# Kernel tuning notes

Measured on AMD Instinct MI355X. Metric: run time of the kernel, lower is better.

Reference implementation:

```python
import jax, jax.numpy as jnp
import numpy as np
import math

IN_DIM = 512
PARAM_DIM = 512
OUT_DIM = 2048
GROUPS = 4
COMPRESS = 4
PLANES = OUT_DIM // COMPRESS          # 512
GROUP_PLANES = PLANES // GROUPS       # 128
ATTN_SCALE = PLANES ** (-0.5)         # note: full planes, as in the source
N, L = 16, 1024
M = L  # required by sv.reshape(N, planes, L)


def equal_linear(x, w, b, in_dim):
    # EqualLinear: F.linear(x, w * (1/sqrt(in_dim)) * lr_mul, bias * lr_mul), lr_mul=1
    scale = 1.0 / math.sqrt(in_dim)
    return jnp.einsum('nlc,oc->nlo', x, w * scale) + b


def setup_inputs() -> dict:
    key = jax.random.key(0)
    ks = jax.random.split(key, 8)
    return {
        'attention': jax.random.normal(ks[0], (N, L, IN_DIM), dtype=jnp.float32),
        'op_param': jax.random.normal(ks[1], (N, M, PARAM_DIM), dtype=jnp.float32),
        'q_w': jax.random.normal(ks[2], (PLANES, PARAM_DIM), dtype=jnp.float32),
        'q_b': jnp.zeros((PLANES,), dtype=jnp.float32),
        'k_w': jax.random.normal(ks[3], (PLANES, IN_DIM), dtype=jnp.float32),
        'k_b': jnp.zeros((PLANES,), dtype=jnp.float32),
        'v_w': jax.random.normal(ks[4], (PLANES, IN_DIM), dtype=jnp.float32),
        'v_b': jnp.zeros((PLANES,), dtype=jnp.float32),
        'proj_w': jax.random.normal(ks[5], (OUT_DIM, PLANES), dtype=jnp.float32),
        'proj_b': jnp.zeros((OUT_DIM,), dtype=jnp.float32),
    }


def reference(attention, op_param, q_w, q_b, k_w, k_b, v_w, v_b, proj_w, proj_b):
    n, l, _ = attention.shape
    m = op_param.shape[1]
    # q/k/v: (N, T, planes) -> (N, groups, group_planes, T)
    q = equal_linear(op_param, q_w, q_b, PARAM_DIM).reshape(n, m, GROUPS, GROUP_PLANES).transpose(0, 2, 3, 1)
    k = equal_linear(attention, k_w, k_b, IN_DIM).reshape(n, l, GROUPS, GROUP_PLANES).transpose(0, 2, 3, 1)
    v = equal_linear(attention, v_w, v_b, IN_DIM).reshape(n, l, GROUPS, GROUP_PLANES).transpose(0, 2, 3, 1)
    # scores: (N, groups, M, L)
    qk = jnp.einsum('ngdm,ngdl->ngml', q, k) * ATTN_SCALE
    sim = jax.nn.softmax(qk, axis=3)
    # sv: (N, groups, group_planes, M)
    sv = jnp.einsum('ngml,ngdl->ngdm', sim, v)
    # (N, planes, L) -> (N, L, planes); valid because M == L
    stacked = sv.reshape(n, PLANES, l).transpose(0, 2, 1)
    out = equal_linear(stacked, proj_w, proj_b, PLANES)
    return out
```

## Files before the change

kernel.cpp:

```cpp
#include <hip/hip_runtime.h>
#include <hip/hip_bf16.h>

#define NB 16
#define TT 1024
#define CC 512
#define PP 512
#define GG 4
#define DD 128
#define OO 2048

#define SCL 0.04419417382415922f

typedef __attribute__((ext_vector_type(8))) short short8;
typedef __attribute__((ext_vector_type(4))) float floatx4;
#define MFMA(a, b, c) __builtin_amdgcn_mfma_f32_16x16x32_bf16((a), (b), (c), 0, 0, 0)

static __device__ __forceinline__ float bf2f(unsigned short u) {
  union { unsigned int i; float f; } v; v.i = ((unsigned int)u) << 16; return v.f;
}
static __device__ __forceinline__ unsigned short f2bf(float f) {
  __hip_bfloat16 h = __float2bfloat16(f);
  return *reinterpret_cast<unsigned short*>(&h);
}
static __device__ __forceinline__ ushort4 pack4(float4 v) {
  ushort4 o; o.x = f2bf(v.x); o.y = f2bf(v.y); o.z = f2bf(v.z); o.w = f2bf(v.w); return o;
}

template <int VLAY>
__global__ __launch_bounds__(256) void k_proj(
    const float* __restrict__ x, const float* __restrict__ w,
    const float* __restrict__ b, unsigned short* __restrict__ y) {
  __shared__ unsigned short Aw[128][32];
  __shared__ unsigned short Xw[128][32];
  const int n  = blockIdx.z;
  const int p0 = blockIdx.y * 128;
  const int t0 = blockIdx.x * 128;
  const int tid  = threadIdx.x;
  const int wave = tid >> 6, lane = tid & 63;
  const int l15  = lane & 15, quad = lane >> 4;
  const int wm = (wave >> 1) * 64, wn = (wave & 1) * 64;
  const int srow = tid >> 3, scol = (tid & 7) * 4;
  const float* xn = x + (size_t)n * TT * CC;
  floatx4 acc[4][4] = {};

  for (int k0 = 0; k0 < CC; k0 += 32) {
    float4 aw[4], ax[4];
#pragma unroll
    for (int q = 0; q < 4; ++q) {
      aw[q] = *reinterpret_cast<const float4*>(w  + (size_t)(p0 + srow + q * 32) * CC + k0 + scol);
      ax[q] = *reinterpret_cast<const float4*>(xn + (size_t)(t0 + srow + q * 32) * CC + k0 + scol);
    }
    __syncthreads();
#pragma unroll
    for (int q = 0; q < 4; ++q) {
      *reinterpret_cast<ushort4*>(&Aw[srow + q * 32][scol]) = pack4(aw[q]);
      *reinterpret_cast<ushort4*>(&Xw[srow + q * 32][scol]) = pack4(ax[q]);
    }
    __syncthreads();
    short8 af[4], bx[4];
#pragma unroll
    for (int mt = 0; mt < 4; ++mt)
      af[mt] = *reinterpret_cast<const short8*>(&Aw[wm + mt * 16 + l15][quad * 8]);
#pragma unroll
    for (int nt = 0; nt < 4; ++nt)
      bx[nt] = *reinterpret_cast<const short8*>(&Xw[wn + nt * 16 + l15][quad * 8]);
#pragma unroll
    for (int mt = 0; mt < 4; ++mt)
#pragma unroll
      for (int nt = 0; nt < 4; ++nt)
        acc[mt][nt] = MFMA(af[mt], bx[nt], acc[mt][nt]);
  }

#pragma unroll
  for (int mt = 0; mt < 4; ++mt) {
    const int pb = p0 + wm + mt * 16 + quad * 4;
    const float4 bias = *reinterpret_cast<const float4*>(b + pb);
    const float bb[4] = {bias.x, bias.y, bias.z, bias.w};
#pragma unroll
    for (int nt = 0; nt < 4; ++nt) {
      const int tc = t0 + wn + nt * 16 + l15;
      if (VLAY == 0) {
        ushort4 o;
        o.x = f2bf(acc[mt][nt][0] * SCL + bb[0]);
        o.y = f2bf(acc[mt][nt][1] * SCL + bb[1]);
        o.z = f2bf(acc[mt][nt][2] * SCL + bb[2]);
        o.w = f2bf(acc[mt][nt][3] * SCL + bb[3]);
        *reinterpret_cast<ushort4*>(y + ((size_t)n * TT + tc) * PP + pb) = o;
      } else {
#pragma unroll
        for (int r = 0; r < 4; ++r)
          y[((size_t)n * PP + pb + r) * TT + tc] = f2bf(acc[mt][nt][r] * SCL + bb[r]);
      }
    }
  }
}

__global__ __launch_bounds__(256, 2) void k_attn(
    const unsigned short* __restrict__ Q,
    const unsigned short* __restrict__ K,
    const unsigned short* __restrict__ V,
    unsigned short* __restrict__ SV) {
  __shared__ unsigned short Sc[32][1032];
  __shared__ float rowinv[32];
  const int lin = blockIdx.x;
  const int wu  = (lin >> 3) | ((lin & 7) << 8);
  const int m0 = (wu & 31) * 32;
  const int g  = (wu >> 5) & 3;
  const int n  = wu >> 7;
  const int tid  = threadIdx.x;
  const int wave = tid >> 6, lane = tid & 63;
  const int l15  = lane & 15, quad = lane >> 4;

  const unsigned short* Qn = Q + (size_t)n * TT * PP;
  const unsigned short* Kn = K + (size_t)n * TT * PP;
  const unsigned short* Vn = V + ((size_t)n * PP + g * DD) * TT;

  short8 aq[2][4];
#pragma unroll
  for (int mt = 0; mt < 2; ++mt)
#pragma unroll
    for (int ds = 0; ds < 4; ++ds)
      aq[mt][ds] = *reinterpret_cast<const short8*>(
          Qn + (size_t)(m0 + mt * 16 + l15) * PP + g * DD + ds * 32 + quad * 8);

  auto kload = [&](short8 (&dst)[4][4], int base_l) {
#pragma unroll
    for (int ds = 0; ds < 4; ++ds)
#pragma unroll
      for (int j = 0; j < 4; ++j)
        dst[ds][j] = *reinterpret_cast<const short8*>(
            Kn + (size_t)(base_l + (wave * 4 + j) * 16 + l15) * PP +
            g * DD + ds * 32 + quad * 8);
  };
  auto kcomp = [&](const short8 (&bk)[4][4], int base_l) {
    floatx4 acc[2][4] = {};
#pragma unroll
    for (int ds = 0; ds < 4; ++ds)
#pragma unroll
      for (int j = 0; j < 4; ++j) {
        acc[0][j] = MFMA(aq[0][ds], bk[ds][j], acc[0][j]);
        acc[1][j] = MFMA(aq[1][ds], bk[ds][j], acc[1][j]);
      }
#pragma unroll
    for (int mt = 0; mt < 2; ++mt)
#pragma unroll
      for (int j = 0; j < 4; ++j) {
        const int lc = base_l + (wave * 4 + j) * 16 + l15;
#pragma unroll
        for (int r = 0; r < 4; ++r)
          Sc[mt * 16 + quad * 4 + r][lc] = f2bf(acc[mt][j][r] * SCL);
      }
  };

  short8 bkA[4][4], bkB[4][4];
  kload(bkA, 0);
  kload(bkB, 256);
  kcomp(bkA, 0);
  kload(bkA, 512);
  kcomp(bkB, 256);
  kload(bkB, 768);
  kcomp(bkA, 512);
  kcomp(bkB, 768);
  __syncthreads();

  {
    const int mi = tid >> 3;
    const int j  = tid & 7;
    unsigned short* row = &Sc[mi][0];
    float mx = -1e30f;
#pragma unroll
    for (int i = 0; i < 16; ++i) {
      short8 u = *reinterpret_cast<const short8*>(&row[(i * 8 + j) * 8]);
      float a0 = fmaxf(bf2f((unsigned short)u[0]), bf2f((unsigned short)u[1]));
      float a1 = fmaxf(bf2f((unsigned short)u[2]), bf2f((unsigned short)u[3]));
      float a2 = fmaxf(bf2f((unsigned short)u[4]), bf2f((unsigned short)u[5]));
      float a3 = fmaxf(bf2f((unsigned short)u[6]), bf2f((unsigned short)u[7]));
      mx = fmaxf(mx, fmaxf(fmaxf(a0, a1), fmaxf(a2, a3)));
    }
#pragma unroll
    for (int off = 4; off; off >>= 1) mx = fmaxf(mx, __shfl_xor(mx, off, 8));
    float sum = 0.f;
#pragma unroll
    for (int i = 0; i < 16; ++i) {
      short8 u = *reinterpret_cast<short8*>(&row[(i * 8 + j) * 8]);
      short8 o;
      float s0 = 0.f, s1 = 0.f;
#pragma unroll
      for (int e = 0; e < 8; e += 2) {
        float e0 = __expf(bf2f((unsigned short)u[e])     - mx);
        float e1 = __expf(bf2f((unsigned short)u[e + 1]) - mx);
        s0 += e0; s1 += e1;
        o[e]     = (short)f2bf(e0);
        o[e + 1] = (short)f2bf(e1);
      }
      sum += s0 + s1;
      *reinterpret_cast<short8*>(&row[(i * 8 + j) * 8]) = o;
    }
#pragma unroll
    for (int off = 4; off; off >>= 1) sum += __shfl_xor(sum, off, 8);
    if (j == 0) rowinv[mi] = 1.f / sum;
  }
  __syncthreads();

  floatx4 av[2][2] = {};
  auto vload = [&](short8 (&dst)[2], int ls) {
#pragma unroll
    for (int a = 0; a < 2; ++a)
      dst[a] = *reinterpret_cast<const short8*>(
          Vn + (size_t)(wave * 32 + a * 16 + l15) * TT + ls * 32 + quad * 8);
  };
  auto vstep = [&](const short8 (&va)[2], int ls) {
    short8 bp[2];
#pragma unroll
    for (int mt = 0; mt < 2; ++mt)
      bp[mt] = *reinterpret_cast<const short8*>(&Sc[mt * 16 + l15][ls * 32 + quad * 8]);
#pragma unroll
    for (int a = 0; a < 2; ++a)
#pragma unroll
      for (int mt = 0; mt < 2; ++mt)
        av[a][mt] = MFMA(va[a], bp[mt], av[a][mt]);
  };

  short8 va0[2], va1[2], va2[2], va3[2];
  vload(va0, 0); vload(va1, 1); vload(va2, 2); vload(va3, 3);
#pragma unroll
  for (int ls = 0; ls < 32; ls += 4) {
    vstep(va0, ls);     if (ls + 4 < 32) vload(va0, ls + 4);
    vstep(va1, ls + 1); if (ls + 5 < 32) vload(va1, ls + 5);
    vstep(va2, ls + 2); if (ls + 6 < 32) vload(va2, ls + 6);
    vstep(va3, ls + 3); if (ls + 7 < 32) vload(va3, ls + 7);
  }

#pragma unroll
  for (int a = 0; a < 2; ++a) {
    const int pb = g * DD + wave * 32 + a * 16 + quad * 4;
#pragma unroll
    for (int mt = 0; mt < 2; ++mt) {
      const float inv = rowinv[mt * 16 + l15];
      ushort4 o;
      o.x = f2bf(av[a][mt][0] * inv);
      o.y = f2bf(av[a][mt][1] * inv);
      o.z = f2bf(av[a][mt][2] * inv);
      o.w = f2bf(av[a][mt][3] * inv);
      *reinterpret_cast<ushort4*>(
          SV + ((size_t)n * TT + m0 + mt * 16 + l15) * PP + pb) = o;
    }
  }
}

__global__ __launch_bounds__(256) void k_out(
    const unsigned short* __restrict__ SVp, const float* __restrict__ w,
    const float* __restrict__ b, float* __restrict__ out) {
  __shared__ unsigned short Wt[128][32];
  __shared__ unsigned short St[128][32];
  const int n  = blockIdx.z;
  const int o0 = blockIdx.y * 128;
  const int t0 = blockIdx.x * 128;
  const int tid  = threadIdx.x;
  const int wave = tid >> 6, lane = tid & 63;
  const int l15  = lane & 15, quad = lane >> 4;
  const int wm = (wave >> 1) * 64, wn = (wave & 1) * 64;
  const int srow = tid >> 3, scol = (tid & 7) * 4;
  const unsigned short* SVn = SVp + (size_t)n * TT * PP;
  floatx4 acc[4][4] = {};

  for (int k0 = 0; k0 < PP; k0 += 32) {
    float4 awf[4];
    ushort4 us[4];
#pragma unroll
    for (int q = 0; q < 4; ++q) {
      awf[q] = *reinterpret_cast<const float4*>(w + (size_t)(o0 + srow + q * 32) * PP + k0 + scol);
      us[q]  = *reinterpret_cast<const ushort4*>(SVn + (size_t)(t0 + srow + q * 32) * PP + k0 + scol);
    }
    __syncthreads();
#pragma unroll
    for (int q = 0; q < 4; ++q) {
      *reinterpret_cast<ushort4*>(&Wt[srow + q * 32][scol]) = pack4(awf[q]);
      *reinterpret_cast<ushort4*>(&St[srow + q * 32][scol]) = us[q];
    }
    __syncthreads();
    short8 af[4], bs[4];
#pragma unroll
    for (int mt = 0; mt < 4; ++mt)
      af[mt] = *reinterpret_cast<const short8*>(&Wt[wm + mt * 16 + l15][quad * 8]);
#pragma unroll
    for (int nt = 0; nt < 4; ++nt)
      bs[nt] = *reinterpret_cast<const short8*>(&St[wn + nt * 16 + l15][quad * 8]);
#pragma unroll
    for (int mt = 0; mt < 4; ++mt)
#pragma unroll
      for (int nt = 0; nt < 4; ++nt)
        acc[mt][nt] = MFMA(af[mt], bs[nt], acc[mt][nt]);
  }

#pragma unroll
  for (int mt = 0; mt < 4; ++mt) {
    const int ob = o0 + wm + mt * 16 + quad * 4;
    const float4 bias = *reinterpret_cast<const float4*>(b + ob);
    const float bb[4] = {bias.x, bias.y, bias.z, bias.w};
#pragma unroll
    for (int nt = 0; nt < 4; ++nt) {
      const int tc = t0 + wn + nt * 16 + l15;
      float4 o;
      o.x = acc[mt][nt][0] * SCL + bb[0];
      o.y = acc[mt][nt][1] * SCL + bb[1];
      o.z = acc[mt][nt][2] * SCL + bb[2];
      o.w = acc[mt][nt][3] * SCL + bb[3];
      *reinterpret_cast<float4*>(out + ((size_t)n * TT + tc) * OO + ob) = o;
    }
  }
}

extern "C" void kernel_launch(void* const* d_in, const int* in_sizes, int n_in,
                              void* d_out, int out_size, void* d_ws, size_t ws_size,
                              hipStream_t stream) {
  (void)in_sizes; (void)n_in; (void)out_size; (void)ws_size;
  const float* attention = (const float*)d_in[0];
  const float* op_param  = (const float*)d_in[1];
  const float* q_w = (const float*)d_in[2];
  const float* q_b = (const float*)d_in[3];
  const float* k_w = (const float*)d_in[4];
  const float* k_b = (const float*)d_in[5];
  const float* v_w = (const float*)d_in[6];
  const float* v_b = (const float*)d_in[7];
  const float* proj_w = (const float*)d_in[8];
  const float* proj_b = (const float*)d_in[9];
  float* out = (float*)d_out;

  const size_t NPT = (size_t)NB * PP * TT;
  unsigned short* scratch = (unsigned short*)d_out;
  unsigned short* Qw  = scratch;
  unsigned short* Kw  = scratch + NPT;
  unsigned short* Vw  = scratch + 2 * NPT;
  unsigned short* SVw = (unsigned short*)d_ws;

  dim3 blk(256);
  dim3 gp(TT / 128, PP / 128, NB);
  k_proj<0><<<gp, blk, 0, stream>>>(op_param,  q_w, q_b, Qw);
  k_proj<0><<<gp, blk, 0, stream>>>(attention, k_w, k_b, Kw);
  k_proj<1><<<gp, blk, 0, stream>>>(attention, v_w, v_b, Vw);
  k_attn<<<dim3(2048), blk, 0, stream>>>(Qw, Kw, Vw, SVw);
  k_out<<<dim3(TT / 128, OO / 128, NB), blk, 0, stream>>>(SVw, proj_w, proj_b, out);
}
```

Measured before the change: 447.1 us.

## Enlarge attention tile to 64 query rows with 512-thread blocks

The attention kernel now handles 64 query rows per block with 8 waves instead of 32 rows with 4 waves. This doubles reuse of each loaded K/V fragment across query rows and halves the grid. The K loop now covers all 1024 keys in two 512-key chunks. The float-to-bf16 conversion is replaced by a manual round-to-nearest-even bit trick. In exchange, register pressure rises sharply under the 512,2 launch bounds, which risks spills, and the 132 KB shared score buffer limits occupancy to one block per CU.

Measured after the change: 418.3 us. -6.4%, faster.

```diff
diff --git a/kernel.cpp b/kernel.cpp
--- a/kernel.cpp
+++ b/kernel.cpp
@@ -19,8 +19,9 @@
   union { unsigned int i; float f; } v; v.i = ((unsigned int)u) << 16; return v.f;
 }
 static __device__ __forceinline__ unsigned short f2bf(float f) {
-  __hip_bfloat16 h = __float2bfloat16(f);
-  return *reinterpret_cast<unsigned short*>(&h);
+  union { float f; unsigned int i; } v; v.f = f;
+  unsigned int r = (v.i + 0x7fffu + ((v.i >> 16) & 1u)) >> 16;
+  return (unsigned short)r;
 }
 static __device__ __forceinline__ ushort4 pack4(float4 v) {
   ushort4 o; o.x = f2bf(v.x); o.y = f2bf(v.y); o.z = f2bf(v.z); o.w = f2bf(v.w); return o;
@@ -95,18 +96,18 @@
   }
 }
 
-__global__ __launch_bounds__(256, 2) void k_attn(
+__global__ __launch_bounds__(512, 2) void k_attn(
     const unsigned short* __restrict__ Q,
     const unsigned short* __restrict__ K,
     const unsigned short* __restrict__ V,
     unsigned short* __restrict__ SV) {
-  __shared__ unsigned short Sc[32][1032];
-  __shared__ float rowinv[32];
+  __shared__ unsigned short Sc[64][1032];
+  __shared__ float rowinv[64];
   const int lin = blockIdx.x;
-  const int wu  = (lin >> 3) | ((lin & 7) << 8);
-  const int m0 = (wu & 31) * 32;
-  const int g  = (wu >> 5) & 3;
-  const int n  = wu >> 7;
+  const int wu  = (lin >> 3) | ((lin & 7) << 7);
+  const int m0 = (wu & 15) * 64;
+  const int g  = (wu >> 4) & 3;
+  const int n  = wu >> 6;
   const int tid  = threadIdx.x;
   const int wave = tid >> 6, lane = tid & 63;
   const int l15  = lane & 15, quad = lane >> 4;
@@ -115,9 +116,9 @@
   const unsigned short* Kn = K + (size_t)n * TT * PP;
   const unsigned short* Vn = V + ((size_t)n * PP + g * DD) * TT;
 
-  short8 aq[2][4];
-#pragma unroll
-  for (int mt = 0; mt < 2; ++mt)
+  short8 aq[4][4];
+#pragma unroll
+  for (int mt = 0; mt < 4; ++mt)
 #pragma unroll
     for (int ds = 0; ds < 4; ++ds)
       aq[mt][ds] = *reinterpret_cast<const short8*>(
@@ -133,16 +134,16 @@
             g * DD + ds * 32 + quad * 8);
   };
   auto kcomp = [&](const short8 (&bk)[4][4], int base_l) {
-    floatx4 acc[2][4] = {};
+    floatx4 acc[4][4] = {};
 #pragma unroll
     for (int ds = 0; ds < 4; ++ds)
 #pragma unroll
-      for (int j = 0; j < 4; ++j) {
-        acc[0][j] = MFMA(aq[0][ds], bk[ds][j], acc[0][j]);
-        acc[1][j] = MFMA(aq[1][ds], bk[ds][j], acc[1][j]);
-      }
-#pragma unroll
-    for (int mt = 0; mt < 2; ++mt)
+      for (int j = 0; j < 4; ++j)
+#pragma unroll
+        for (int mt = 0; mt < 4; ++mt)
+          acc[mt][j] = MFMA(aq[mt][ds], bk[ds][j], acc[mt][j]);
+#pragma unroll
+    for (int mt = 0; mt < 4; ++mt)
 #pragma unroll
       for (int j = 0; j < 4; ++j) {
         const int lc = base_l + (wave * 4 + j) * 16 + l15;
@@ -154,13 +155,9 @@
 
   short8 bkA[4][4], bkB[4][4];
   kload(bkA, 0);
-  kload(bkB, 256);
+  kload(bkB, 512);
   kcomp(bkA, 0);
-  kload(bkA, 512);
-  kcomp(bkB, 256);
-  kload(bkB, 768);
-  kcomp(bkA, 512);
-  kcomp(bkB, 768);
+  kcomp(bkB, 512);
   __syncthreads();
 
   {
@@ -202,49 +199,39 @@
   }
   __syncthreads();
 
-  floatx4 av[2][2] = {};
-  auto vload = [&](short8 (&dst)[2], int ls) {
-#pragma unroll
-    for (int a = 0; a < 2; ++a)
-      dst[a] = *reinterpret_cast<const short8*>(
-          Vn + (size_t)(wave * 32 + a * 16 + l15) * TT + ls * 32 + quad * 8);
+  floatx4 av[4] = {};
+  auto vload = [&](int ls) {
+    return *reinterpret_cast<const short8*>(
+        Vn + (size_t)(wave * 16 + l15) * TT + ls * 32 + quad * 8);
   };
-  auto vstep = [&](const short8 (&va)[2], int ls) {
-    short8 bp[2];
-#pragma unroll
-    for (int mt = 0; mt < 2; ++mt)
-      bp[mt] = *reinterpret_cast<const short8*>(&Sc[mt * 16 + l15][ls * 32 + quad * 8]);
-#pragma unroll
-    for (int a = 0; a < 2; ++a)
-#pragma unroll
-      for (int mt = 0; mt < 2; ++mt)
-        av[a][mt] = MFMA(va[a], bp[mt], av[a][mt]);
+  auto vstep = [&](short8 va, int ls) {
+#pragma unroll
+    for (int mt = 0; mt < 4; ++mt) {
+      short8 bp = *reinterpret_cast<const short8*>(&Sc[mt * 16 + l15][ls * 32 + quad * 8]);
+      av[mt] = MFMA(va, bp, av[mt]);
+    }
   };
 
-  short8 va0[2], va1[2], va2[2], va3[2];
-  vload(va0, 0); vload(va1, 1); vload(va2, 2); vload(va3, 3);
+  short8 va0 = vload(0), va1 = vload(1), va2 = vload(2), va3 = vload(3);
 #pragma unroll
   for (int ls = 0; ls < 32; ls += 4) {
-    vstep(va0, ls);     if (ls + 4 < 32) vload(va0, ls + 4);
-    vstep(va1, ls + 1); if (ls + 5 < 32) vload(va1, ls + 5);
-    vstep(va2, ls + 2); if (ls + 6 < 32) vload(va2, ls + 6);
-    vstep(va3, ls + 3); if (ls + 7 < 32) vload(va3, ls + 7);
-  }
-
-#pragma unroll
-  for (int a = 0; a < 2; ++a) {
-    const int pb = g * DD + wave * 32 + a * 16 + quad * 4;
-#pragma unroll
-    for (int mt = 0; mt < 2; ++mt) {
-      const float inv = rowinv[mt * 16 + l15];
-      ushort4 o;
-      o.x = f2bf(av[a][mt][0] * inv);
-      o.y = f2bf(av[a][mt][1] * inv);
-      o.z = f2bf(av[a][mt][2] * inv);
-      o.w = f2bf(av[a][mt][3] * inv);
-      *reinterpret_cast<ushort4*>(
-          SV + ((size_t)n * TT + m0 + mt * 16 + l15) * PP + pb) = o;
-    }
+    vstep(va0, ls);     if (ls + 4 < 32) va0 = vload(ls + 4);
+    vstep(va1, ls + 1); if (ls + 5 < 32) va1 = vload(ls + 5);
+    vstep(va2, ls + 2); if (ls + 6 < 32) va2 = vload(ls + 6);
+    vstep(va3, ls + 3); if (ls + 7 < 32) va3 = vload(ls + 7);
+  }
+
+  const int pb = g * DD + wave * 16 + quad * 4;
+#pragma unroll
+  for (int mt = 0; mt < 4; ++mt) {
+    const float inv = rowinv[mt * 16 + l15];
+    ushort4 o;
+    o.x = f2bf(av[mt][0] * inv);
+    o.y = f2bf(av[mt][1] * inv);
+    o.z = f2bf(av[mt][2] * inv);
+    o.w = f2bf(av[mt][3] * inv);
+    *reinterpret_cast<ushort4*>(
+        SV + ((size_t)n * TT + m0 + mt * 16 + l15) * PP + pb) = o;
   }
 }
 
@@ -339,6 +326,6 @@
   k_proj<0><<<gp, blk, 0, stream>>>(op_param,  q_w, q_b, Qw);
   k_proj<0><<<gp, blk, 0, stream>>>(attention, k_w, k_b, Kw);
   k_proj<1><<<gp, blk, 0, stream>>>(attention, v_w, v_b, Vw);
-  k_attn<<<dim3(2048), blk, 0, stream>>>(Qw, Kw, Vw, SVw);
+  k_attn<<<dim3(1024), dim3(512), 0, stream>>>(Qw, Kw, Vw, SVw);
   k_out<<<dim3(TT / 128, OO / 128, NB), blk, 0, stream>>>(SVw, proj_w, proj_b, out);
 }
```
